# Kernel tuning notes

Hardware: AMD Instinct MI355X
Metric: run time of the kernel (lower is better)

## Reference

```python
import jax, jax.numpy as jnp
import numpy as np

B, DIM, N = 4, 256, 2048
DIM_CTX, M = 256, 2048
HEADS, DIM_HEAD = 8, 64
DIM_INNER = HEADS * DIM_HEAD  # 512
EPS = 1e-12  # matches F.normalize eps


def setup_inputs() -> dict:
    key = jax.random.key(0)
    ks = jax.random.split(key, 8)
    return {
        "fmap": jax.random.normal(ks[0], (B, DIM, N), dtype=jnp.float32),
        "context": jax.random.normal(ks[1], (B, DIM_CTX, M), dtype=jnp.float32),
        "mask": jax.random.randint(ks[2], (B, M), 0, 2) > 0,
        "gamma": jnp.ones((DIM, 1), dtype=jnp.float32),
        "gamma_ctx": jnp.ones((DIM_CTX, 1), dtype=jnp.float32),
        "Wq": jax.random.normal(ks[3], (DIM_INNER, DIM), dtype=jnp.float32) * (DIM ** -0.5),
        "Wkv": jax.random.normal(ks[4], (2 * DIM_INNER, DIM_CTX), dtype=jnp.float32) * (DIM_CTX ** -0.5),
        "Wout": jax.random.normal(ks[5], (DIM, DIM_INNER), dtype=jnp.float32) * (DIM_INNER ** -0.5),
    }


def channel_rmsnorm(x, gamma):
    # F.normalize(x, dim=1) * sqrt(dim) * gamma ; x: [b, c, n], gamma: [c, 1]
    scale = x.shape[1] ** 0.5
    norm = jnp.sqrt(jnp.sum(x * x, axis=1, keepdims=True))
    normed = x / jnp.maximum(norm, EPS)
    return normed * scale * gamma[None]


def reference(fmap, context, mask, gamma, gamma_ctx, Wq, Wkv, Wout):
    h, d = HEADS, DIM_HEAD
    attn_scale = d ** -0.5

    fmap_n = channel_rmsnorm(fmap, gamma)          # [b, dim, n]
    ctx_n = channel_rmsnorm(context, gamma_ctx)    # [b, dim_ctx, m]

    # 1x1 Conv1d == matmul over channels
    q = jnp.einsum('oc,bcn->bon', Wq, fmap_n)      # [b, h*d, n]
    kv = jnp.einsum('oc,bcm->bom', Wkv, ctx_n)     # [b, 2*h*d, m]
    k, v = jnp.split(kv, 2, axis=1)

    # [b, h*d, n] -> [b, h, n, d]
    def to_heads(t):
        b, _, nn = t.shape
        return t.reshape(b, h, d, nn).transpose(0, 1, 3, 2)

    q, k, v = to_heads(q), to_heads(k), to_heads(v)

    # L2-distance attention: sim = -||q_i - k_j||_2 * scale
    q2 = jnp.sum(q * q, axis=-1)                   # [b, h, n]
    k2 = jnp.sum(k * k, axis=-1)                   # [b, h, m]
    qk = jnp.einsum('bhid,bhjd->bhij', q, k)       # [b, h, n, m]
    d2 = jnp.maximum(q2[..., :, None] + k2[..., None, :] - 2.0 * qk, 0.0)
    dist = jnp.sqrt(jnp.maximum(d2, EPS))
    sim = -dist * attn_scale

    neg_max = -jnp.finfo(sim.dtype).max
    sim = jnp.where(mask[:, None, None, :], sim, neg_max)

    attn = jax.nn.softmax(sim, axis=-1)            # [b, h, n, m]
    out = jnp.einsum('bhij,bhjd->bhid', attn, v)   # [b, h, n, d]
    out = out.transpose(0, 1, 3, 2).reshape(out.shape[0], h * d, -1)  # [b, h*d, n]
    return jnp.einsum('oc,bcn->bon', Wout, out)    # [b, dim, n]
```

## Files before the change

### kernel.cpp

```cpp
#include <hip/hip_runtime.h>
#include <hip/hip_bf16.h>

#define B_ 4
#define DIM_ 256
#define N_ 2048
#define M_ 2048
#define HEADS_ 8
#define DHEAD_ 64
#define DINNER_ 512

typedef __attribute__((ext_vector_type(8))) short short8;
typedef __attribute__((ext_vector_type(4))) short short4v;
typedef __attribute__((ext_vector_type(4))) float floatx4;
typedef __attribute__((ext_vector_type(4))) _Float16 half4;
typedef __attribute__((ext_vector_type(8))) _Float16 half8;

#if defined(__has_builtin)
#if __has_builtin(__builtin_amdgcn_global_load_lds)
#define HAS_DMA 1
#endif
#endif

typedef __attribute__((address_space(1))) const void gvoid_t;
typedef __attribute__((address_space(3))) void lvoid_t;

#define CQ_ 0.18033688011112042f
#define NEG2CQ_ (-0.36067376022224084f)
#define EPS2_ 3.25213893e-14f

__device__ inline short bf16r(float x) {
  unsigned u = __float_as_uint(x);
  unsigned r = (u + 0x7fffu + ((u >> 16) & 1u)) >> 16;
  return (short)r;
}
__device__ inline float bf2f(short b) {
  return __uint_as_float(((unsigned)(unsigned short)b) << 16);
}

__global__ __launch_bounds__(256) void preproc_kernel(
    const float* __restrict__ Wq, const float* __restrict__ Wkv,
    const float* __restrict__ Wout, const float* __restrict__ gamma,
    const float* __restrict__ gctx, short* __restrict__ whi,
    short* __restrict__ wlo, const float* __restrict__ xf,
    const float* __restrict__ xc, short* __restrict__ xtf,
    short* __restrict__ xtc) {
  const int bid = blockIdx.x;
  const int tid = threadIdx.x;

  __shared__ float red[4][64];
  __shared__ float scl[64];
  __shared__ float t[64][65];

  if (bid < 768) {
    const int y = bid >> 8;
    const int gsz[3] = {32768, 65536, 32768};
    const int goff[3] = {0, 131072, 393216};
    int gidx = (bid & 255) * 256 + tid;
    if (gidx >= gsz[y]) return;
    const float* W = (y == 0) ? Wq : (y == 1) ? Wkv : Wout;
    const int cmask = (y == 2) ? 511 : 255;
    int e0 = gidx * 4;
    int c = e0 & cmask;
    float4 wv = *(const float4*)&W[e0];
    if (y < 2) {
      const float* g = (y == 0) ? gamma : gctx;
      float4 g4 = *(const float4*)&g[c];
      wv.x *= g4.x; wv.y *= g4.y; wv.z *= g4.z; wv.w *= g4.w;
    }
    float vv[4] = {wv.x, wv.y, wv.z, wv.w};
    short4v hi, lo;
#pragma unroll
    for (int e = 0; e < 4; ++e) {
      short hb = bf16r(vv[e]);
      hi[e] = hb;
      lo[e] = bf16r(vv[e] - bf2f(hb));
    }
    *(short4v*)&whi[goff[y] + e0] = hi;
    *(short4v*)&wlo[goff[y] + e0] = lo;
    return;
  }

  const int cid = bid - 768;
  const int NN = 2048;
  const int z = cid >> 7;
  const int b = (cid >> 5) & 3;
  const int xblk = cid & 31;
  const float* x = (z == 0) ? xf : xc;
  short* xt = (z == 0) ? xtf : xtc;
  const int tx = tid & 63, ty = tid >> 6;
  const int n0 = xblk * 64, n = n0 + tx;
  const float* xb = x + (size_t)b * 256 * NN;

  float ssq = 0.f;
  for (int c = ty; c < 256; c += 4) {
    float v = xb[(size_t)c * NN + n];
    ssq += v * v;
  }
  red[ty][tx] = ssq;
  __syncthreads();
  if (ty == 0) {
    float s = red[0][tx] + red[1][tx] + red[2][tx] + red[3][tx];
    scl[tx] = 16.0f / fmaxf(sqrtf(s), 1e-12f);
  }
  const int row = tid >> 2, cg = tid & 3;
  for (int c0 = 0; c0 < 256; c0 += 64) {
    __syncthreads();
    for (int cc = ty; cc < 64; cc += 4) t[cc][tx] = xb[(size_t)(c0 + cc) * NN + n];
    __syncthreads();
    float sc = scl[row];
    short8 o0v, o1v;
#pragma unroll
    for (int e = 0; e < 8; ++e) {
      o0v[e] = bf16r(t[cg * 16 + e][row] * sc);
      o1v[e] = bf16r(t[cg * 16 + 8 + e][row] * sc);
    }
    size_t base = ((size_t)b * NN + n0 + row) * 256 + c0 + cg * 16;
    *(short8*)&xt[base] = o0v;
    *(short8*)&xt[base + 8] = o1v;
  }
}

__global__ __launch_bounds__(256) void qkv_gemm_kernel(
    const short* __restrict__ whi, const short* __restrict__ wlo,
    const short* __restrict__ fmap_t, const short* __restrict__ ctx_t,
    short* __restrict__ qb, short* __restrict__ kc, _Float16* __restrict__ vc,
    const int* __restrict__ maskp, float* __restrict__ k2m) {
  const int b = blockIdx.z;
  const int y = blockIdx.y;
  const bool isq = (y < 4);
  const int o0 = (isq ? y : y - 4) * 128;
  const int n0 = blockIdx.x * 128;
  const short* Wh = whi + (isq ? 0 : 131072);
  const short* Wl = wlo + (isq ? 0 : 131072);
  const short* Xt = isq ? fmap_t : ctx_t;

  const int tid = threadIdx.x;
  const int w = tid >> 6, l = tid & 63, quad = l >> 4, l15 = l & 15;
  const int wo = (w >> 1) * 64, wn = (w & 1) * 64;

  __shared__ __align__(16) short Wa[2][128][40];
  __shared__ __align__(16) short Xb[128][40];

  floatx4 acc[4][4];
#pragma unroll
  for (int ot = 0; ot < 4; ++ot)
#pragma unroll
    for (int nt = 0; nt < 4; ++nt)
#pragma unroll
      for (int r = 0; r < 4; ++r) acc[ot][nt][r] = 0.f;

  for (int c0 = 0; c0 < 256; c0 += 32) {
    __syncthreads();
#pragma unroll
    for (int it = 0; it < 2; ++it) {
      int lin = tid + it * 256;
      int row = lin >> 2, sg = (lin & 3) * 8;
      size_t src = (size_t)(o0 + row) * 256 + c0 + sg;
      *(short8*)&Wa[0][row][sg] = *(const short8*)&Wh[src];
      *(short8*)&Wa[1][row][sg] = *(const short8*)&Wl[src];
    }
#pragma unroll
    for (int it = 0; it < 2; ++it) {
      int lin = tid + it * 256;
      int nn = lin >> 2, sg = (lin & 3) * 8;
      *(short8*)&Xb[nn][sg] =
          *(const short8*)&Xt[((size_t)b * 2048 + n0 + nn) * 256 + c0 + sg];
    }
    __syncthreads();

    short8 ah[4], al[4], bx[4];
#pragma unroll
    for (int ot = 0; ot < 4; ++ot) {
      ah[ot] = *(const short8*)&Wa[0][wo + 16 * ot + l15][8 * quad];
      al[ot] = *(const short8*)&Wa[1][wo + 16 * ot + l15][8 * quad];
    }
#pragma unroll
    for (int nt = 0; nt < 4; ++nt)
      bx[nt] = *(const short8*)&Xb[wn + 16 * nt + l15][8 * quad];
#pragma unroll
    for (int ot = 0; ot < 4; ++ot)
#pragma unroll
      for (int nt = 0; nt < 4; ++nt) {
        acc[ot][nt] =
            __builtin_amdgcn_mfma_f32_16x16x32_bf16(al[ot], bx[nt], acc[ot][nt], 0, 0, 0);
        acc[ot][nt] =
            __builtin_amdgcn_mfma_f32_16x16x32_bf16(ah[ot], bx[nt], acc[ot][nt], 0, 0, 0);
      }
  }

  if (isq) {
#pragma unroll
    for (int nt = 0; nt < 4; ++nt) {
      int n = n0 + wn + 16 * nt + l15;
      size_t base = ((size_t)b * 2048 + n) * 512;
#pragma unroll
      for (int ot = 0; ot < 4; ++ot) {
        int o = o0 + wo + 16 * ot + 4 * quad;
        short4v pk;
#pragma unroll
        for (int r = 0; r < 4; ++r) pk[r] = bf16r(CQ_ * acc[ot][nt][r]);
        *(short4v*)&qb[base + o] = pk;
      }
    }
  } else if (o0 < 512) {
    const int head = (o0 + wo) >> 6;
    const int bh = b * 8 + head;
    float k2p[4] = {0.f, 0.f, 0.f, 0.f};
#pragma unroll
    for (int nt = 0; nt < 4; ++nt) {
      int m = n0 + wn + 16 * nt + l15;
      int chunk = m >> 6, mrow = m & 63;
      size_t tbase = (((size_t)bh * 32 + chunk) * 64 + mrow) * 64;
      int sw = mrow & 7;
#pragma unroll
      for (int ot = 0; ot < 4; ++ot) {
        int d0 = 16 * ot + 4 * quad;
        short4v pk;
#pragma unroll
        for (int r = 0; r < 4; ++r) {
          short pv = bf16r(NEG2CQ_ * acc[ot][nt][r]);
          pk[r] = pv;
          float kr = bf2f(pv);
          k2p[nt] += kr * kr;
        }
        *(short4v*)&kc[tbase + (size_t)(((d0 >> 3) ^ sw) << 3) + (d0 & 7)] = pk;
      }
    }
#pragma unroll
    for (int nt = 0; nt < 4; ++nt) {
      float s = k2p[nt];
      s += __shfl_xor(s, 16);
      s += __shfl_xor(s, 32);
      if (quad == 0) {
        int m = n0 + wn + 16 * nt + l15;
        int mv = maskp[b * 2048 + m];
        k2m[(size_t)bh * 2048 + m] = mv ? 0.25f * s : __builtin_inff();
      }
    }
  } else {
    const int chv = o0 - 512 + wo;
    const int bh = b * 8 + (chv >> 6);
#pragma unroll
    for (int nt = 0; nt < 4; ++nt) {
      int j = n0 + wn + 16 * nt + l15;
      int chunk = j >> 6, jr = j & 63;
      int jrem = jr & 31;
      int colp = 32 * (jr >> 5) + ((jrem >> 2) & 3) * 8 + (jrem >> 4) * 4 +
                 (jrem & 3);
      size_t cbase = ((size_t)bh * 32 + chunk) * 4096;
#pragma unroll
      for (int ot = 0; ot < 4; ++ot)
#pragma unroll
        for (int r = 0; r < 4; ++r) {
          int drow = (chv + 16 * ot + 4 * quad + r) & 63;
          vc[cbase + drow * 64 + (((colp >> 3) ^ (drow & 7)) << 3) +
             (colp & 7)] = (_Float16)acc[ot][nt][r];
        }
    }
  }
}

__global__ __launch_bounds__(512, 8) void attn_kernel(
    const short* __restrict__ qb, const short* __restrict__ kc,
    const _Float16* __restrict__ vc, const float* __restrict__ k2m,
    short* __restrict__ attn_t) {
  const int bid = blockIdx.x;
  const int rr = bid & 7, qq = bid >> 3;
  const int bh = rr * 4 + (qq >> 5);
  const int iblk = qq & 31;
  const int h = bh & 7, b = bh >> 3;
  const int i0 = iblk * 64;

  const int tid = threadIdx.x;
  const int w = tid >> 6, l = tid & 63, quad = l >> 4, l15 = l & 15;
  const int wr = w >> 1, jh = w & 1;

  __shared__ __align__(16) short sbuf[2][2][4096];

  const short* qrow =
      qb + ((size_t)b * 2048 + i0 + 16 * wr + l15) * 512 + h * 64;
  const short* kcb = kc + (size_t)bh * 32 * 4096;
  const _Float16* vcb = vc + (size_t)bh * 32 * 4096;
  const float* k2b = k2m + (size_t)bh * 2048;

  short8 qa0 = *(const short8*)&qrow[8 * quad];
  short8 qa1 = *(const short8*)&qrow[32 + 8 * quad];
  float q2p = 0.f;
#pragma unroll
  for (int jj = 0; jj < 8; ++jj) {
    float f0 = bf2f(qa0[jj]), f1 = bf2f(qa1[jj]);
    q2p += f0 * f0 + f1 * f1;
  }
  q2p += __shfl_xor(q2p, 16);
  q2p += __shfl_xor(q2p, 32);
  const float q2c = q2p;

  floatx4 accO[4];
#pragma unroll
  for (int dt = 0; dt < 4; ++dt)
#pragma unroll
    for (int r = 0; r < 4; ++r) accO[dt][r] = 0.f;
  float lsum = 0.f;

  const int sx = l15 & 7;

  auto stage = [&](int c, int p) {
    const short* ks = kcb + (size_t)c * 4096 + w * 512 + l * 8;
    const _Float16* vs = vcb + (size_t)c * 4096 + w * 512 + l * 8;
#ifdef HAS_DMA
    __builtin_amdgcn_global_load_lds((gvoid_t*)ks,
                                     (lvoid_t*)&sbuf[0][p][w * 512], 16, 0, 0);
    __builtin_amdgcn_global_load_lds((gvoid_t*)vs,
                                     (lvoid_t*)&sbuf[1][p][w * 512], 16, 0, 0);
#else
    *(short8*)&sbuf[0][p][w * 512 + l * 8] = *(const short8*)ks;
    *(half8*)&((_Float16*)sbuf[1][p])[w * 512 + l * 8] = *(const half8*)vs;
#endif
  };

  float4 k2pf0 = *(const float4*)&k2b[jh * 32 + 4 * quad];
  float4 k2pf1 = *(const float4*)&k2b[jh * 32 + 16 + 4 * quad];

  stage(0, 0);
  for (int c = 0; c < 32; ++c) {
    __syncthreads();
    if (c < 31) stage(c + 1, (c + 1) & 1);
    const int p = c & 1;

    float4 k2c0 = k2pf0, k2c1 = k2pf1;
    if (c < 31) {
      k2pf0 = *(const float4*)&k2b[(c + 1) * 64 + jh * 32 + 4 * quad];
      k2pf1 = *(const float4*)&k2b[(c + 1) * 64 + jh * 32 + 16 + 4 * quad];
    }

    half8 pb;
#pragma unroll
    for (int jt = 0; jt < 2; ++jt) {
      float4 k2v = jt ? k2c1 : k2c0;
      const short* kr = &sbuf[0][p][(jh * 32 + 16 * jt + l15) * 64];
      short8 k0 = *(const short8*)&kr[(quad ^ sx) << 3];
      short8 k1 = *(const short8*)&kr[((quad + 4) ^ sx) << 3];
      floatx4 a;
      a[0] = q2c + k2v.x;
      a[1] = q2c + k2v.y;
      a[2] = q2c + k2v.z;
      a[3] = q2c + k2v.w;
      __builtin_amdgcn_s_setprio(1);
      a = __builtin_amdgcn_mfma_f32_16x16x32_bf16(k0, qa0, a, 0, 0, 0);
      a = __builtin_amdgcn_mfma_f32_16x16x32_bf16(k1, qa1, a, 0, 0, 0);
      __builtin_amdgcn_s_setprio(0);
#pragma unroll
      for (int r = 0; r < 4; ++r) {
        float s = __builtin_amdgcn_sqrtf(fmaxf(a[r], EPS2_));
        float pv = __builtin_amdgcn_exp2f(-s);
        lsum += pv;
        pb[4 * jt + r] = (_Float16)pv;
      }
    }

    __builtin_amdgcn_s_setprio(1);
#pragma unroll
    for (int dt = 0; dt < 4; ++dt) {
      const _Float16* vr = (const _Float16*)&sbuf[1][p][(16 * dt + l15) * 64];
      half8 hh = *(const half8*)&vr[((quad + 4 * jh) ^ sx) << 3];
      accO[dt] =
          __builtin_amdgcn_mfma_f32_16x16x32_f16(hh, pb, accO[dt], 0, 0, 0);
    }
    __builtin_amdgcn_s_setprio(0);
  }

  __syncthreads();
  float* scr = (float*)sbuf;
  const int sidx = (wr * 64 + l) * 17;
  if (jh) {
#pragma unroll
    for (int dt = 0; dt < 4; ++dt)
#pragma unroll
      for (int r = 0; r < 4; ++r) scr[sidx + dt * 4 + r] = accO[dt][r];
    scr[sidx + 16] = lsum;
  }
  __syncthreads();
  if (!jh) {
#pragma unroll
    for (int dt = 0; dt < 4; ++dt)
#pragma unroll
      for (int r = 0; r < 4; ++r) accO[dt][r] += scr[sidx + dt * 4 + r];
    lsum += scr[sidx + 16];
    lsum += __shfl_xor(lsum, 16);
    lsum += __shfl_xor(lsum, 32);
    float rl = 1.0f / lsum;
    size_t base = ((size_t)b * 2048 + i0 + 16 * wr + l15) * 512 + h * 64;
#pragma unroll
    for (int dt = 0; dt < 4; ++dt) {
      short4v pk;
#pragma unroll
      for (int r = 0; r < 4; ++r) pk[r] = bf16r(accO[dt][r] * rl);
      *(short4v*)&attn_t[base + 16 * dt + 4 * quad] = pk;
    }
  }
}

__global__ __launch_bounds__(256) void outproj_kernel(
    const short* __restrict__ whi, const short* __restrict__ wlo,
    const short* __restrict__ Xt, float* __restrict__ Yf) {
  const int b = blockIdx.z;
  const int n0 = blockIdx.x * 128;
  const int o0 = blockIdx.y * 64;
  const int tid = threadIdx.x;
  const int w = tid >> 6, l = tid & 63, quad = l >> 4, l15 = l & 15;
  const int wo = (w >> 1) * 32, wn = (w & 1) * 64;

  __shared__ __align__(16) short Wa[2][64][40];
  __shared__ __align__(16) short Xb[128][40];

  floatx4 acc[2][4];
#pragma unroll
  for (int ot = 0; ot < 2; ++ot)
#pragma unroll
    for (int nt = 0; nt < 4; ++nt)
#pragma unroll
      for (int r = 0; r < 4; ++r) acc[ot][nt][r] = 0.f;

  for (int c0 = 0; c0 < 512; c0 += 32) {
    __syncthreads();
    {
      int row = tid >> 2, sg = (tid & 3) * 8;
      size_t src = (size_t)(o0 + row) * 512 + c0 + sg;
      *(short8*)&Wa[0][row][sg] = *(const short8*)&whi[src];
      *(short8*)&Wa[1][row][sg] = *(const short8*)&wlo[src];
    }
#pragma unroll
    for (int it = 0; it < 2; ++it) {
      int lin = tid + it * 256;
      int nn = lin >> 2, sg = (lin & 3) * 8;
      *(short8*)&Xb[nn][sg] =
          *(const short8*)&Xt[((size_t)b * 2048 + n0 + nn) * 512 + c0 + sg];
    }
    __syncthreads();

    short8 ah[2], al[2], bx[4];
#pragma unroll
    for (int ot = 0; ot < 2; ++ot) {
      ah[ot] = *(const short8*)&Wa[0][wo + 16 * ot + l15][8 * quad];
      al[ot] = *(const short8*)&Wa[1][wo + 16 * ot + l15][8 * quad];
    }
#pragma unroll
    for (int nt = 0; nt < 4; ++nt)
      bx[nt] = *(const short8*)&Xb[wn + 16 * nt + l15][8 * quad];
#pragma unroll
    for (int ot = 0; ot < 2; ++ot)
#pragma unroll
      for (int nt = 0; nt < 4; ++nt) {
        acc[ot][nt] =
            __builtin_amdgcn_mfma_f32_16x16x32_bf16(al[ot], bx[nt], acc[ot][nt], 0, 0, 0);
        acc[ot][nt] =
            __builtin_amdgcn_mfma_f32_16x16x32_bf16(ah[ot], bx[nt], acc[ot][nt], 0, 0, 0);
      }
  }

#pragma unroll
  for (int ot = 0; ot < 2; ++ot)
#pragma unroll
    for (int r = 0; r < 4; ++r) {
      int o = o0 + wo + 16 * ot + 4 * quad + r;
#pragma unroll
      for (int nt = 0; nt < 4; ++nt)
        Yf[((size_t)b * 256 + o) * 2048 + n0 + wn + 16 * nt + l15] =
            acc[ot][nt][r];
    }
}

extern "C" void kernel_launch(void* const* d_in, const int* in_sizes, int n_in,
                              void* d_out, int out_size, void* d_ws,
                              size_t ws_size, hipStream_t stream) {
  const float* fmap = (const float*)d_in[0];
  const float* context = (const float*)d_in[1];
  const int* mask = (const int*)d_in[2];
  const float* gamma = (const float*)d_in[3];
  const float* gamma_ctx = (const float*)d_in[4];
  const float* Wq = (const float*)d_in[5];
  const float* Wkv = (const float*)d_in[6];
  const float* Wout = (const float*)d_in[7];
  float* out = (float*)d_out;

  char* ws = (char*)d_ws;
  short* fmap_t = (short*)ws;
  short* ctx_t = fmap_t + 2097152;
  short* qb = ctx_t + 2097152;
  short* kc = qb + 4194304;
  _Float16* vc = (_Float16*)(kc + 4194304);
  short* attn_t = (short*)(vc + 4194304);
  float* k2m = (float*)(attn_t + 4194304);
  short* whi = (short*)(k2m + 65536);
  short* wlo = whi + 524288;

  preproc_kernel<<<dim3(1024), 256, 0, stream>>>(
      Wq, Wkv, Wout, gamma, gamma_ctx, whi, wlo, fmap, context, fmap_t, ctx_t);
  qkv_gemm_kernel<<<dim3(16, 12, B_), 256, 0, stream>>>(
      whi, wlo, fmap_t, ctx_t, qb, kc, vc, mask, k2m);
  attn_kernel<<<dim3(1024), 512, 0, stream>>>(qb, kc, vc, k2m, attn_t);
  outproj_kernel<<<dim3(16, 4, B_), 256, 0, stream>>>(whi + 393216,
                                                      wlo + 393216, attn_t,
                                                      out);
}
```

Measured before the change: 211.6 us.

## Stage K/V epilogue through LDS for coalesced stores; load k2 inline

Result: faster. 195.6 us (-7.6%).

```diff
diff --git a/kernel.cpp b/kernel.cpp
--- a/kernel.cpp
+++ b/kernel.cpp
@@ -138,8 +138,9 @@
   const int w = tid >> 6, l = tid & 63, quad = l >> 4, l15 = l & 15;
   const int wo = (w >> 1) * 64, wn = (w & 1) * 64;
 
-  __shared__ __align__(16) short Wa[2][128][40];
-  __shared__ __align__(16) short Xb[128][40];
+  __shared__ __align__(16) char smem[36864];
+  short (*Wa)[128][40] = (short (*)[128][40])smem;
+  short (*Xb)[40] = (short (*)[40])(smem + 20480);
 
   floatx4 acc[4][4];
 #pragma unroll
@@ -205,12 +206,13 @@
   } else if (o0 < 512) {
     const int head = (o0 + wo) >> 6;
     const int bh = b * 8 + head;
+    const int chunk = (n0 + wn) >> 6;
+    __syncthreads();
+    short (*kt)[72] = (short (*)[72])(smem + w * 9216);
     float k2p[4] = {0.f, 0.f, 0.f, 0.f};
 #pragma unroll
     for (int nt = 0; nt < 4; ++nt) {
-      int m = n0 + wn + 16 * nt + l15;
-      int chunk = m >> 6, mrow = m & 63;
-      size_t tbase = (((size_t)bh * 32 + chunk) * 64 + mrow) * 64;
+      int mrow = 16 * nt + l15;
       int sw = mrow & 7;
 #pragma unroll
       for (int ot = 0; ot < 4; ++ot) {
@@ -223,8 +225,15 @@
           float kr = bf2f(pv);
           k2p[nt] += kr * kr;
         }
-        *(short4v*)&kc[tbase + (size_t)(((d0 >> 3) ^ sw) << 3) + (d0 & 7)] = pk;
+        *(short4v*)&kt[mrow][(((d0 >> 3) ^ sw) << 3) + (d0 & 7)] = pk;
       }
+    }
+    size_t tbase = ((size_t)bh * 32 + chunk) * 4096;
+#pragma unroll
+    for (int it = 0; it < 8; ++it) {
+      int mr = 8 * it + (l >> 3);
+      int c8 = (l & 7) * 8;
+      *(short8*)&kc[tbase + mr * 64 + c8] = *(const short8*)&kt[mr][c8];
     }
 #pragma unroll
     for (int nt = 0; nt < 4; ++nt) {
@@ -240,22 +249,30 @@
   } else {
     const int chv = o0 - 512 + wo;
     const int bh = b * 8 + (chv >> 6);
+    const int chunk = (n0 + wn) >> 6;
+    __syncthreads();
+    _Float16 (*vt)[72] = (_Float16 (*)[72])(smem + w * 9216);
 #pragma unroll
     for (int nt = 0; nt < 4; ++nt) {
-      int j = n0 + wn + 16 * nt + l15;
-      int chunk = j >> 6, jr = j & 63;
+      int jr = 16 * nt + l15;
       int jrem = jr & 31;
       int colp = 32 * (jr >> 5) + ((jrem >> 2) & 3) * 8 + (jrem >> 4) * 4 +
                  (jrem & 3);
-      size_t cbase = ((size_t)bh * 32 + chunk) * 4096;
 #pragma unroll
       for (int ot = 0; ot < 4; ++ot)
 #pragma unroll
         for (int r = 0; r < 4; ++r) {
-          int drow = (chv + 16 * ot + 4 * quad + r) & 63;
-          vc[cbase + drow * 64 + (((colp >> 3) ^ (drow & 7)) << 3) +
-             (colp & 7)] = (_Float16)acc[ot][nt][r];
+          int drow = (16 * ot + 4 * quad + r) & 63;
+          vt[drow][(((colp >> 3) ^ (drow & 7)) << 3) + (colp & 7)] =
+              (_Float16)acc[ot][nt][r];
         }
+    }
+    size_t cbase = ((size_t)bh * 32 + chunk) * 4096;
+#pragma unroll
+    for (int it = 0; it < 8; ++it) {
+      int dr = 8 * it + (l >> 3);
+      int c8 = (l & 7) * 8;
+      *(half8*)&vc[cbase + dr * 64 + c8] = *(const half8*)&vt[dr][c8];
     }
   }
 }
@@ -318,25 +335,16 @@
 #endif
   };
 
-  float4 k2pf0 = *(const float4*)&k2b[jh * 32 + 4 * quad];
-  float4 k2pf1 = *(const float4*)&k2b[jh * 32 + 16 + 4 * quad];
-
   stage(0, 0);
   for (int c = 0; c < 32; ++c) {
     __syncthreads();
     if (c < 31) stage(c + 1, (c + 1) & 1);
     const int p = c & 1;
 
-    float4 k2c0 = k2pf0, k2c1 = k2pf1;
-    if (c < 31) {
-      k2pf0 = *(const float4*)&k2b[(c + 1) * 64 + jh * 32 + 4 * quad];
-      k2pf1 = *(const float4*)&k2b[(c + 1) * 64 + jh * 32 + 16 + 4 * quad];
-    }
-
     half8 pb;
 #pragma unroll
     for (int jt = 0; jt < 2; ++jt) {
-      float4 k2v = jt ? k2c1 : k2c0;
+      float4 k2v = *(const float4*)&k2b[c * 64 + jh * 32 + 16 * jt + 4 * quad];
       const short* kr = &sbuf[0][p][(jh * 32 + 16 * jt + l15) * 64];
       short8 k0 = *(const short8*)&kr[(quad ^ sx) << 3];
       short8 k1 = *(const short8*)&kr[((quad + 4) ^ sx) << 3];
```
